# Kernel tuning notes

Hardware: AMD Instinct MI355X
Metric: run time of the kernel (lower is better)

Reference implementation:

```python
import jax, jax.numpy as jnp
import numpy as np

DIM = 2048
HID = 5632
ZERO_POINT = 128.0


def _qlinear(x, wq, scale):
    # wq: uint8-style codes stored as int32, shape [out, in]; scale: [out]
    W = (wq.astype(jnp.float32) - ZERO_POINT) * scale[:, None]  # dequant [out, in]
    return jnp.einsum('bsd,hd->bsh', x, W)


def setup_inputs() -> dict:
    key = jax.random.key(0)
    ks = jax.random.split(key, 7)
    B, S = 4, 2048
    # scale chosen so dequantized weights have ~1/sqrt(fan_in) magnitude
    sg = jax.random.uniform(ks[1], (HID,)) * (0.02 / np.sqrt(DIM)) + 1e-4
    su = jax.random.uniform(ks[3], (HID,)) * (0.02 / np.sqrt(DIM)) + 1e-4
    sd = jax.random.uniform(ks[5], (DIM,)) * (0.02 / np.sqrt(HID)) + 1e-4
    return {
        'x': jax.random.normal(ks[0], (B, S, DIM), dtype=jnp.float32),
        'wq_gate': jax.random.randint(ks[2], (HID, DIM), 0, 256, dtype=jnp.int32),
        's_gate': sg,
        'wq_up': jax.random.randint(ks[4], (HID, DIM), 0, 256, dtype=jnp.int32),
        's_up': su,
        'wq_down': jax.random.randint(ks[6], (DIM, HID), 0, 256, dtype=jnp.int32),
        's_down': sd,
    }


def reference(x, wq_gate, s_gate, wq_up, s_up, wq_down, s_down):
    gate = _qlinear(x, wq_gate, s_gate)          # [B, S, HID]
    gate = jax.nn.silu(gate)
    up = _qlinear(x, wq_up, s_up)                # [B, S, HID]
    return _qlinear(gate * up, wq_down, s_down)  # [B, S, DIM]
```

## Files before the change

kernel.cpp:

```cpp
#include <hip/hip_runtime.h>
#include <hip/hip_bf16.h>
#include <stdint.h>

#define DIM 2048
#define HID 5632
#define PDIM 2176

typedef __attribute__((ext_vector_type(8))) short short8;
typedef __attribute__((ext_vector_type(4))) float f32x4;
typedef __attribute__((ext_vector_type(4))) int int4v;
typedef __attribute__((ext_vector_type(4))) unsigned short ushort4v;

__device__ __forceinline__ unsigned short f32_to_bf16_rne(float f) {
    union { float f; unsigned u; } v; v.f = f;
    unsigned u = v.u;
    return (unsigned short)((u + 0x7FFFu + ((u >> 16) & 1u)) >> 16);
}

__device__ __forceinline__ void gload16(const void* g, void* l) {
    __builtin_amdgcn_global_load_lds(
        (const __attribute__((address_space(1))) void*)g,
        (__attribute__((address_space(3))) void*)l,
        16, 0, 0);
}

#define PH_OPEN \
    __builtin_amdgcn_sched_barrier(0); \
    __builtin_amdgcn_s_barrier(); \
    asm volatile("s_waitcnt lgkmcnt(0)" ::: "memory"); \
    __builtin_amdgcn_sched_barrier(0); \
    __builtin_amdgcn_s_setprio(1);
#define PH_CLOSE \
    __builtin_amdgcn_s_setprio(0); \
    __builtin_amdgcn_sched_barrier(0); \
    __builtin_amdgcn_s_barrier(); \
    __builtin_amdgcn_sched_barrier(0);
#define PH_CLOSE_VM(N) \
    __builtin_amdgcn_s_setprio(0); \
    __builtin_amdgcn_sched_barrier(0); \
    asm volatile("s_waitcnt vmcnt(" #N ")" ::: "memory"); \
    __builtin_amdgcn_sched_barrier(0); \
    __builtin_amdgcn_s_barrier(); \
    __builtin_amdgcn_sched_barrier(0);

__global__ void dequant_plain(const int* __restrict__ wq, const float* __restrict__ scale,
                              unsigned short* __restrict__ out, long total, int cols) {
    long n4 = total >> 2;
    long stride = (long)gridDim.x * blockDim.x;
    for (long i = (long)blockIdx.x * blockDim.x + threadIdx.x; i < n4; i += stride) {
        int4v c = ((const int4v*)wq)[i];
        int row = (int)((i << 2) / cols);
        float s = scale[row];
        ushort4v o;
        o.x = f32_to_bf16_rne(((float)c.x - 128.0f) * s);
        o.y = f32_to_bf16_rne(((float)c.y - 128.0f) * s);
        o.z = f32_to_bf16_rne(((float)c.z - 128.0f) * s);
        o.w = f32_to_bf16_rne(((float)c.w - 128.0f) * s);
        ((ushort4v*)out)[i] = o;
    }
}

__global__ void dequant_gateup(const int* __restrict__ wg, const float* __restrict__ sg,
                               const int* __restrict__ wu, const float* __restrict__ su,
                               unsigned short* __restrict__ out) {
    const long n4 = (long)HID * DIM / 4;
    const int CPR = PDIM / 4;
    long stride = (long)gridDim.x * blockDim.x;
    for (long i = (long)blockIdx.x * blockDim.x + threadIdx.x; i < n4; i += stride) {
        int r  = (int)(i >> 9);
        int c4 = (int)(i & 511);
        int rp = ((r >> 4) << 5) + (r & 15);
        float s1 = sg[r], s2 = su[r];
        int4v g = ((const int4v*)wg)[i];
        int4v u = ((const int4v*)wu)[i];
        ushort4v og, ou;
        og.x = f32_to_bf16_rne(((float)g.x - 128.0f) * s1);
        og.y = f32_to_bf16_rne(((float)g.y - 128.0f) * s1);
        og.z = f32_to_bf16_rne(((float)g.z - 128.0f) * s1);
        og.w = f32_to_bf16_rne(((float)g.w - 128.0f) * s1);
        ou.x = f32_to_bf16_rne(((float)u.x - 128.0f) * s2);
        ou.y = f32_to_bf16_rne(((float)u.y - 128.0f) * s2);
        ou.z = f32_to_bf16_rne(((float)u.z - 128.0f) * s2);
        ou.w = f32_to_bf16_rne(((float)u.w - 128.0f) * s2);
        ((ushort4v*)out)[(long)rp * CPR + c4]        = og;
        ((ushort4v*)out)[(long)(rp + 16) * CPR + c4] = ou;
    }
}

__global__ void cast_f32_bf16(const float* __restrict__ in, unsigned short* __restrict__ out, long n) {
    long n4 = n >> 2;
    const int CPR = PDIM / 4;
    long stride = (long)gridDim.x * blockDim.x;
    for (long i = (long)blockIdx.x * blockDim.x + threadIdx.x; i < n4; i += stride) {
        f32x4 v = ((const f32x4*)in)[i];
        int r  = (int)(i >> 9);
        int c4 = (int)(i & 511);
        ushort4v o;
        o.x = f32_to_bf16_rne(v[0]);
        o.y = f32_to_bf16_rne(v[1]);
        o.z = f32_to_bf16_rne(v[2]);
        o.w = f32_to_bf16_rne(v[3]);
        ((ushort4v*)out)[(long)r * CPR + c4] = o;
    }
}


#define GEMM_PROLOGUE_COMMON(Aptr, Bptr, LDA, LDB)                                   \
    const int tid  = threadIdx.x;                                                    \
    const int lane = tid & 63;                                                       \
    const int wid  = tid >> 6;                                                       \
    const int wr   = wid >> 2;                                                       \
    const int wc   = wid & 3;                                                        \
    const int m0   = blockIdx.x << 8;                                                \
    const int n0   = blockIdx.y << 8;                                                \
    const int lr   = lane & 15;                                                      \
    const int kg   = lane >> 4;                                                      \
    const int ck   = ((kg ^ ((lr >> 1) & 3)) << 3);                                  \
    const int aboff = (wr * 128 + lr) * 32;                                          \
    const int bboff = (wc * 64 + lr) * 32;                                           \
    int srow[2], scol[2], sdst[2];                                                   \
    _Pragma("unroll")                                                                \
    for (int l = 0; l < 2; ++l) {                                                    \
        int p = tid + (l << 9);                                                      \
        srow[l] = p >> 2;                                                            \
        scol[l] = (((p & 3) ^ ((p >> 3) & 3)) << 3);                                 \
        sdst[l] = p << 3;                                                            \
    }                                                                                \
    auto STAGE_A = [&](int t, int kh) {                                              \
        if (t < NT) {                                                                \
            unsigned short* dst = As + ((((t & 1) << 1) | kh) << 13);                \
            _Pragma("unroll")                                                        \
            for (int l = 0; l < 2; ++l)                                              \
                gload16(Aptr + (size_t)(m0 + srow[l]) * LDA + (t << 6) + (kh << 5) + scol[l], \
                        dst + sdst[l]);                                              \
        }                                                                            \
    };                                                                               \
    auto STAGE_B = [&](int t, int kh) {                                              \
        if (t < NT) {                                                                \
            unsigned short* dst = Bs + ((((t & 1) << 1) | kh) << 13);                \
            _Pragma("unroll")                                                        \
            for (int l = 0; l < 2; ++l)                                              \
                gload16(Bptr + (size_t)(n0 + srow[l]) * LDB + (t << 6) + (kh << 5) + scol[l], \
                        dst + sdst[l]);                                              \
        }                                                                            \
    };                                                                               \
    f32x4 acc[8][4];                                                                 \
    _Pragma("unroll")                                                                \
    for (int m = 0; m < 8; ++m)                                                      \
        _Pragma("unroll")                                                            \
        for (int n = 0; n < 4; ++n) acc[m][n] = (f32x4){0.f, 0.f, 0.f, 0.f};         \
                            \
    STAGE_A(0, 0); STAGE_B(0, 0);                                                    \
    STAGE_A(0, 1); STAGE_B(0, 1);                                                    \
    STAGE_A(1, 0); STAGE_B(1, 0);                                                    \
    asm volatile("s_waitcnt vmcnt(8)" ::: "memory");                                 \
    __builtin_amdgcn_s_barrier();

#define GEMM_KLOOP_BODY                                                              \
    for (int t = 0; t < NT; ++t) {                                                   \
        const int buf = t & 1;                                                       \
        const unsigned short* a0p = As + ((buf << 1) << 13) + aboff + ck;            \
        const unsigned short* a1p = As + (((buf << 1) | 1) << 13) + aboff + ck;      \
        const unsigned short* b0p = Bs + ((buf << 1) << 13) + bboff + ck;            \
        const unsigned short* b1p = Bs + (((buf << 1) | 1) << 13) + bboff + ck;      \
                                            \
        short8 b0[4], aL0[4];                                                        \
        _Pragma("unroll")                                                            \
        for (int n = 0; n < 4; ++n) b0[n] = *(const short8*)(b0p + (n << 9));        \
        _Pragma("unroll")                                                            \
        for (int m = 0; m < 4; ++m) aL0[m] = *(const short8*)(a0p + (m << 9));       \
        STAGE_A(t + 1, 1);                                                           \
        PH_OPEN                                                                      \
        _Pragma("unroll")                                                            \
        for (int m = 0; m < 4; ++m)                                                  \
            _Pragma("unroll")                                                        \
            for (int n = 0; n < 4; ++n)                                              \
                acc[m][n] = __builtin_amdgcn_mfma_f32_16x16x32_bf16(aL0[m], b0[n], acc[m][n], 0, 0, 0); \
        PH_CLOSE                                                                     \
                           \
        short8 aH0[4];                                                               \
        _Pragma("unroll")                                                            \
        for (int m = 0; m < 4; ++m) aH0[m] = *(const short8*)(a0p + ((m + 4) << 9)); \
        STAGE_B(t + 1, 1);                                                           \
        PH_OPEN                                                                      \
        _Pragma("unroll")                                                            \
        for (int m = 0; m < 4; ++m)                                                  \
            _Pragma("unroll")                                                        \
            for (int n = 0; n < 4; ++n)                                              \
                acc[m + 4][n] = __builtin_amdgcn_mfma_f32_16x16x32_bf16(aH0[m], b0[n], acc[m + 4][n], 0, 0, 0); \
        if (t < NT - 1) { PH_CLOSE_VM(8) } else { PH_CLOSE_VM(0) }                   \
                                            \
        short8 b1[4], aL1[4];                                                        \
        _Pragma("unroll")                                                            \
        for (int n = 0; n < 4; ++n) b1[n] = *(const short8*)(b1p + (n << 9));        \
        _Pragma("unroll")                                                            \
        for (int m = 0; m < 4; ++m) aL1[m] = *(const short8*)(a1p + (m << 9));       \
        STAGE_A(t + 2, 0);                                                           \
        PH_OPEN                                                                      \
        _Pragma("unroll")                                                            \
        for (int m = 0; m < 4; ++m)                                                  \
            _Pragma("unroll")                                                        \
            for (int n = 0; n < 4; ++n)                                              \
                acc[m][n] = __builtin_amdgcn_mfma_f32_16x16x32_bf16(aL1[m], b1[n], acc[m][n], 0, 0, 0); \
        PH_CLOSE                                                                     \
                         \
        short8 aH1[4];                                                               \
        _Pragma("unroll")                                                            \
        for (int m = 0; m < 4; ++m) aH1[m] = *(const short8*)(a1p + ((m + 4) << 9)); \
        STAGE_B(t + 2, 0);                                                           \
        PH_OPEN                                                                      \
        _Pragma("unroll")                                                            \
        for (int m = 0; m < 4; ++m)                                                  \
            _Pragma("unroll")                                                        \
            for (int n = 0; n < 4; ++n)                                              \
                acc[m + 4][n] = __builtin_amdgcn_mfma_f32_16x16x32_bf16(aH1[m], b1[n], acc[m + 4][n], 0, 0, 0); \
        if (t < NT - 2) { PH_CLOSE_VM(8) } else { PH_CLOSE_VM(4) }                   \
    }

__global__ __launch_bounds__(512, 1) void gemm_gateup(
    const unsigned short* __restrict__ X,
    const unsigned short* __restrict__ Wp,
    unsigned short* __restrict__ H)
{
    __shared__ __attribute__((aligned(16))) unsigned short As[2 * 2 * 8192];
    __shared__ __attribute__((aligned(16))) unsigned short Bs[2 * 2 * 8192];
    const int NT = DIM / 64;
    GEMM_PROLOGUE_COMMON(X, Wp, PDIM, PDIM)
    GEMM_KLOOP_BODY

    const int lg = lane >> 4;
    #pragma unroll
    for (int m = 0; m < 8; ++m) {
        #pragma unroll
        for (int i = 0; i < 2; ++i) {
            f32x4 g = acc[m][2 * i], u = acc[m][2 * i + 1];
            const int col = (blockIdx.y << 7) + wc * 32 + i * 16 + lr;
            #pragma unroll
            for (int e = 0; e < 4; ++e) {
                const int row = m0 + wr * 128 + m * 16 + lg * 4 + e;
                float gv = g[e];
                float sg = gv / (1.0f + __expf(-gv));
                H[(size_t)row * HID + col] = f32_to_bf16_rne(sg * u[e]);
            }
        }
    }
}

__global__ __launch_bounds__(512, 1) void gemm_down(
    const unsigned short* __restrict__ Hb,
    const unsigned short* __restrict__ Wd,
    float* __restrict__ Out)
{
    __shared__ __attribute__((aligned(16))) unsigned short As[2 * 2 * 8192];
    __shared__ __attribute__((aligned(16))) unsigned short Bs[2 * 2 * 8192];
    const int NT = HID / 64;
    GEMM_PROLOGUE_COMMON(Hb, Wd, HID, HID)
    GEMM_KLOOP_BODY

    const int lg = lane >> 4;
    #pragma unroll
    for (int m = 0; m < 8; ++m) {
        #pragma unroll
        for (int n = 0; n < 4; ++n) {
            const int col = n0 + wc * 64 + n * 16 + lr;
            #pragma unroll
            for (int e = 0; e < 4; ++e) {
                const int row = m0 + wr * 128 + m * 16 + lg * 4 + e;
                Out[(size_t)row * DIM + col] = acc[m][n][e];
            }
        }
    }
}

extern "C" void kernel_launch(void* const* d_in, const int* in_sizes, int n_in,
                              void* d_out, int out_size, void* d_ws, size_t ws_size,
                              hipStream_t stream) {
    const float* x      = (const float*)d_in[0];
    const int* wq_gate  = (const int*)d_in[1];
    const float* s_gate = (const float*)d_in[2];
    const int* wq_up    = (const int*)d_in[3];
    const float* s_up   = (const float*)d_in[4];
    const int* wq_down  = (const int*)d_in[5];
    const float* s_down = (const float*)d_in[6];
    float* out = (float*)d_out;

    const int M = in_sizes[0] / DIM;

    unsigned short* xb  = (unsigned short*)d_ws;
    unsigned short* wgu = xb + (size_t)M * PDIM;
    unsigned short* h   = wgu + (size_t)2 * HID * PDIM;

    cast_f32_bf16<<<2048, 256, 0, stream>>>(x, xb, (long)M * DIM);
    dequant_gateup<<<2048, 256, 0, stream>>>(wq_gate, s_gate, wq_up, s_up, wgu);

    gemm_gateup<<<dim3(M / 256, (2 * HID) / 256), 512, 0, stream>>>(xb, wgu, h);

    dequant_plain<<<2048, 256, 0, stream>>>(wq_down, s_down, wgu, (long)DIM * HID, HID);

    gemm_down<<<dim3(M / 256, DIM / 256), 512, 0, stream>>>(h, wgu, out);
}
```

Baseline: 600.9 us.

## Stage weights as uint8 and dequantize in registers, apply scales in epilogue

Weights are repacked to uint8 codes instead of pre-dequantized bf16. The GEMMs load half as many bytes per B tile into LDS and convert codes to bf16 (code minus zero point) in registers just before the MFMAs. Per-row scales are applied to the accumulators in the epilogue rather than baked into the weights. This cuts weight-repack write traffic and B-tile load bandwidth, at the cost of extra VALU conversion work inside the hot loop and a changed LDS swizzle and waitcnt schedule.

New measurement: 703.3 us. +17.0%, slower.

```diff
diff --git a/kernel.cpp b/kernel.cpp
--- a/kernel.cpp
+++ b/kernel.cpp
@@ -10,6 +10,8 @@
 typedef __attribute__((ext_vector_type(4))) float f32x4;
 typedef __attribute__((ext_vector_type(4))) int int4v;
 typedef __attribute__((ext_vector_type(4))) unsigned short ushort4v;
+typedef __attribute__((ext_vector_type(4))) unsigned char uchar4v;
+typedef __attribute__((ext_vector_type(2))) unsigned int u32x2;
 
 __device__ __forceinline__ unsigned short f32_to_bf16_rne(float f) {
     union { float f; unsigned u; } v; v.f = f;
@@ -24,6 +26,26 @@
         16, 0, 0);
 }
 
+__device__ __forceinline__ short8 deq8(u32x2 raw) {
+    float f[8];
+    #pragma unroll
+    for (int j = 0; j < 2; ++j) {
+        unsigned w = raw[j];
+        f[4*j+0] = (float)(w & 0xffu);
+        f[4*j+1] = (float)((w >> 8) & 0xffu);
+        f[4*j+2] = (float)((w >> 16) & 0xffu);
+        f[4*j+3] = (float)(w >> 24);
+    }
+    union { unsigned u[4]; short8 v; } cv;
+    #pragma unroll
+    for (int j = 0; j < 4; ++j) {
+        float lo = f[2*j]   - 128.0f;
+        float hi = f[2*j+1] - 128.0f;
+        asm("v_cvt_pk_bf16_f32 %0, %1, %2" : "=v"(cv.u[j]) : "v"(lo), "v"(hi));
+    }
+    return cv.v;
+}
+
 #define PH_OPEN \
     __builtin_amdgcn_sched_barrier(0); \
     __builtin_amdgcn_s_barrier(); \
@@ -43,47 +65,37 @@
     __builtin_amdgcn_s_barrier(); \
     __builtin_amdgcn_sched_barrier(0);
 
-__global__ void dequant_plain(const int* __restrict__ wq, const float* __restrict__ scale,
-                              unsigned short* __restrict__ out, long total, int cols) {
+__global__ void repack_plain(const int* __restrict__ wq, unsigned char* __restrict__ out, long total) {
     long n4 = total >> 2;
     long stride = (long)gridDim.x * blockDim.x;
     for (long i = (long)blockIdx.x * blockDim.x + threadIdx.x; i < n4; i += stride) {
         int4v c = ((const int4v*)wq)[i];
-        int row = (int)((i << 2) / cols);
-        float s = scale[row];
-        ushort4v o;
-        o.x = f32_to_bf16_rne(((float)c.x - 128.0f) * s);
-        o.y = f32_to_bf16_rne(((float)c.y - 128.0f) * s);
-        o.z = f32_to_bf16_rne(((float)c.z - 128.0f) * s);
-        o.w = f32_to_bf16_rne(((float)c.w - 128.0f) * s);
-        ((ushort4v*)out)[i] = o;
-    }
-}
-
-__global__ void dequant_gateup(const int* __restrict__ wg, const float* __restrict__ sg,
-                               const int* __restrict__ wu, const float* __restrict__ su,
-                               unsigned short* __restrict__ out) {
+        uchar4v o;
+        o.x = (unsigned char)c.x; o.y = (unsigned char)c.y;
+        o.z = (unsigned char)c.z; o.w = (unsigned char)c.w;
+        ((uchar4v*)out)[i] = o;
+    }
+}
+
+__global__ void repack_gateup(const int* __restrict__ wg, const float* __restrict__ sg,
+                              const int* __restrict__ wu, const float* __restrict__ su,
+                              unsigned char* __restrict__ out, float* __restrict__ sWp) {
     const long n4 = (long)HID * DIM / 4;
-    const int CPR = PDIM / 4;
     long stride = (long)gridDim.x * blockDim.x;
     for (long i = (long)blockIdx.x * blockDim.x + threadIdx.x; i < n4; i += stride) {
         int r  = (int)(i >> 9);
         int c4 = (int)(i & 511);
         int rp = ((r >> 4) << 5) + (r & 15);
-        float s1 = sg[r], s2 = su[r];
         int4v g = ((const int4v*)wg)[i];
         int4v u = ((const int4v*)wu)[i];
-        ushort4v og, ou;
-        og.x = f32_to_bf16_rne(((float)g.x - 128.0f) * s1);
-        og.y = f32_to_bf16_rne(((float)g.y - 128.0f) * s1);
-        og.z = f32_to_bf16_rne(((float)g.z - 128.0f) * s1);
-        og.w = f32_to_bf16_rne(((float)g.w - 128.0f) * s1);
-        ou.x = f32_to_bf16_rne(((float)u.x - 128.0f) * s2);
-        ou.y = f32_to_bf16_rne(((float)u.y - 128.0f) * s2);
-        ou.z = f32_to_bf16_rne(((float)u.z - 128.0f) * s2);
-        ou.w = f32_to_bf16_rne(((float)u.w - 128.0f) * s2);
-        ((ushort4v*)out)[(long)rp * CPR + c4]        = og;
-        ((ushort4v*)out)[(long)(rp + 16) * CPR + c4] = ou;
+        uchar4v og, ou;
+        og.x = (unsigned char)g.x; og.y = (unsigned char)g.y;
+        og.z = (unsigned char)g.z; og.w = (unsigned char)g.w;
+        ou.x = (unsigned char)u.x; ou.y = (unsigned char)u.y;
+        ou.z = (unsigned char)u.z; ou.w = (unsigned char)u.w;
+        *(uchar4v*)(out + (long)rp * PDIM + c4 * 4)        = og;
+        *(uchar4v*)(out + (long)(rp + 16) * PDIM + c4 * 4) = ou;
+        if (c4 == 0) { sWp[rp] = sg[r]; sWp[rp + 16] = su[r]; }
     }
 }
 
@@ -105,7 +117,7 @@
 }
 
 
-#define GEMM_PROLOGUE_COMMON(Aptr, Bptr, LDA, LDB)                                   \
+#define GEMM_PROLOGUE_COMMON(Aptr, Bptr, Sc, LDA, LDBB)                              \
     const int tid  = threadIdx.x;                                                    \
     const int lane = tid & 63;                                                       \
     const int wid  = tid >> 6;                                                       \
@@ -117,7 +129,8 @@
     const int kg   = lane >> 4;                                                      \
     const int ck   = ((kg ^ ((lr >> 1) & 3)) << 3);                                  \
     const int aboff = (wr * 128 + lr) * 32;                                          \
-    const int bboff = (wc * 64 + lr) * 32;                                           \
+    const int bcol8 = ((((kg >> 1) ^ ((lr >> 2) & 1)) << 4) | ((kg & 1) << 3));      \
+    const int bboff = (wc * 64 + lr) * 32 + bcol8;                                   \
     int srow[2], scol[2], sdst[2];                                                   \
     _Pragma("unroll")                                                                \
     for (int l = 0; l < 2; ++l) {                                                    \
@@ -126,6 +139,8 @@
         scol[l] = (((p & 3) ^ ((p >> 3) & 3)) << 3);                                 \
         sdst[l] = p << 3;                                                            \
     }                                                                                \
+    const int brow = tid >> 1;                                                       \
+    const int bsc  = (((tid & 1) ^ ((brow >> 2) & 1)) << 4);                         \
     auto STAGE_A = [&](int t, int kh) {                                              \
         if (t < NT) {                                                                \
             unsigned short* dst = As + ((((t & 1) << 1) | kh) << 13);                \
@@ -137,23 +152,23 @@
     };                                                                               \
     auto STAGE_B = [&](int t, int kh) {                                              \
         if (t < NT) {                                                                \
-            unsigned short* dst = Bs + ((((t & 1) << 1) | kh) << 13);                \
-            _Pragma("unroll")                                                        \
-            for (int l = 0; l < 2; ++l)                                              \
-                gload16(Bptr + (size_t)(n0 + srow[l]) * LDB + (t << 6) + (kh << 5) + scol[l], \
-                        dst + sdst[l]);                                              \
+            unsigned char* dst = Bs + ((((t & 1) << 1) | kh) << 13);                 \
+            gload16(Bptr + (size_t)(n0 + brow) * LDBB + (t << 6) + (kh << 5) + bsc,  \
+                    dst + (tid << 4));                                               \
         }                                                                            \
     };                                                                               \
+    float sB[4];                                                                     \
+    _Pragma("unroll")                                                                \
+    for (int n = 0; n < 4; ++n) sB[n] = Sc[n0 + wc * 64 + n * 16 + lr];              \
     f32x4 acc[8][4];                                                                 \
     _Pragma("unroll")                                                                \
     for (int m = 0; m < 8; ++m)                                                      \
         _Pragma("unroll")                                                            \
         for (int n = 0; n < 4; ++n) acc[m][n] = (f32x4){0.f, 0.f, 0.f, 0.f};         \
-                            \
     STAGE_A(0, 0); STAGE_B(0, 0);                                                    \
     STAGE_A(0, 1); STAGE_B(0, 1);                                                    \
     STAGE_A(1, 0); STAGE_B(1, 0);                                                    \
-    asm volatile("s_waitcnt vmcnt(8)" ::: "memory");                                 \
+    asm volatile("s_waitcnt vmcnt(6)" ::: "memory");                                 \
     __builtin_amdgcn_s_barrier();
 
 #define GEMM_KLOOP_BODY                                                              \
@@ -161,23 +176,25 @@
         const int buf = t & 1;                                                       \
         const unsigned short* a0p = As + ((buf << 1) << 13) + aboff + ck;            \
         const unsigned short* a1p = As + (((buf << 1) | 1) << 13) + aboff + ck;      \
-        const unsigned short* b0p = Bs + ((buf << 1) << 13) + bboff + ck;            \
-        const unsigned short* b1p = Bs + (((buf << 1) | 1) << 13) + bboff + ck;      \
-                                            \
-        short8 b0[4], aL0[4];                                                        \
-        _Pragma("unroll")                                                            \
-        for (int n = 0; n < 4; ++n) b0[n] = *(const short8*)(b0p + (n << 9));        \
+        const unsigned char*  bq0 = Bs + ((buf << 1) << 13) + bboff;                 \
+        const unsigned char*  bq1 = Bs + (((buf << 1) | 1) << 13) + bboff;           \
+                                        \
+        u32x2 b0r[4]; short8 aL0[4], b0[4];                                          \
+        _Pragma("unroll")                                                            \
+        for (int n = 0; n < 4; ++n) b0r[n] = *(const u32x2*)(bq0 + (n << 9));        \
         _Pragma("unroll")                                                            \
         for (int m = 0; m < 4; ++m) aL0[m] = *(const short8*)(a0p + (m << 9));       \
         STAGE_A(t + 1, 1);                                                           \
         PH_OPEN                                                                      \
         _Pragma("unroll")                                                            \
+        for (int n = 0; n < 4; ++n) b0[n] = deq8(b0r[n]);                            \
+        _Pragma("unroll")                                                            \
         for (int m = 0; m < 4; ++m)                                                  \
             _Pragma("unroll")                                                        \
             for (int n = 0; n < 4; ++n)                                              \
                 acc[m][n] = __builtin_amdgcn_mfma_f32_16x16x32_bf16(aL0[m], b0[n], acc[m][n], 0, 0, 0); \
         PH_CLOSE                                                                     \
-                           \
+                                                 \
         short8 aH0[4];                                                               \
         _Pragma("unroll")                                                            \
         for (int m = 0; m < 4; ++m) aH0[m] = *(const short8*)(a0p + ((m + 4) << 9)); \
@@ -188,22 +205,24 @@
             _Pragma("unroll")                                                        \
             for (int n = 0; n < 4; ++n)                                              \
                 acc[m + 4][n] = __builtin_amdgcn_mfma_f32_16x16x32_bf16(aH0[m], b0[n], acc[m + 4][n], 0, 0, 0); \
-        if (t < NT - 1) { PH_CLOSE_VM(8) } else { PH_CLOSE_VM(0) }                   \
-                                            \
-        short8 b1[4], aL1[4];                                                        \
-        _Pragma("unroll")                                                            \
-        for (int n = 0; n < 4; ++n) b1[n] = *(const short8*)(b1p + (n << 9));        \
+        if (t < NT - 1) { PH_CLOSE_VM(6) } else { PH_CLOSE_VM(0) }                   \
+                                        \
+        u32x2 b1r[4]; short8 aL1[4], b1[4];                                          \
+        _Pragma("unroll")                                                            \
+        for (int n = 0; n < 4; ++n) b1r[n] = *(const u32x2*)(bq1 + (n << 9));        \
         _Pragma("unroll")                                                            \
         for (int m = 0; m < 4; ++m) aL1[m] = *(const short8*)(a1p + (m << 9));       \
         STAGE_A(t + 2, 0);                                                           \
         PH_OPEN                                                                      \
         _Pragma("unroll")                                                            \
+        for (int n = 0; n < 4; ++n) b1[n] = deq8(b1r[n]);                            \
+        _Pragma("unroll")                                                            \
         for (int m = 0; m < 4; ++m)                                                  \
             _Pragma("unroll")                                                        \
             for (int n = 0; n < 4; ++n)                                              \
                 acc[m][n] = __builtin_amdgcn_mfma_f32_16x16x32_bf16(aL1[m], b1[n], acc[m][n], 0, 0, 0); \
         PH_CLOSE                                                                     \
-                         \
+                                                 \
         short8 aH1[4];                                                               \
         _Pragma("unroll")                                                            \
         for (int m = 0; m < 4; ++m) aH1[m] = *(const short8*)(a1p + ((m + 4) << 9)); \
@@ -214,18 +233,19 @@
             _Pragma("unroll")                                                        \
             for (int n = 0; n < 4; ++n)                                              \
                 acc[m + 4][n] = __builtin_amdgcn_mfma_f32_16x16x32_bf16(aH1[m], b1[n], acc[m + 4][n], 0, 0, 0); \
-        if (t < NT - 2) { PH_CLOSE_VM(8) } else { PH_CLOSE_VM(4) }                   \
+        if (t < NT - 2) { PH_CLOSE_VM(6) } else { PH_CLOSE_VM(3) }                   \
     }
 
 __global__ __launch_bounds__(512, 1) void gemm_gateup(
     const unsigned short* __restrict__ X,
-    const unsigned short* __restrict__ Wp,
+    const unsigned char* __restrict__ Wp8,
+    const float* __restrict__ sWp,
     unsigned short* __restrict__ H)
 {
     __shared__ __attribute__((aligned(16))) unsigned short As[2 * 2 * 8192];
-    __shared__ __attribute__((aligned(16))) unsigned short Bs[2 * 2 * 8192];
+    __shared__ __attribute__((aligned(16))) unsigned char  Bs[2 * 2 * 8192];
     const int NT = DIM / 64;
-    GEMM_PROLOGUE_COMMON(X, Wp, PDIM, PDIM)
+    GEMM_PROLOGUE_COMMON(X, Wp8, sWp, PDIM, PDIM)
     GEMM_KLOOP_BODY
 
     const int lg = lane >> 4;
@@ -238,9 +258,10 @@
             #pragma unroll
             for (int e = 0; e < 4; ++e) {
                 const int row = m0 + wr * 128 + m * 16 + lg * 4 + e;
-                float gv = g[e];
+                float gv = g[e] * sB[2 * i];
+                float uv = u[e] * sB[2 * i + 1];
                 float sg = gv / (1.0f + __expf(-gv));
-                H[(size_t)row * HID + col] = f32_to_bf16_rne(sg * u[e]);
+                H[(size_t)row * HID + col] = f32_to_bf16_rne(sg * uv);
             }
         }
     }
@@ -248,13 +269,14 @@
 
 __global__ __launch_bounds__(512, 1) void gemm_down(
     const unsigned short* __restrict__ Hb,
-    const unsigned short* __restrict__ Wd,
+    const unsigned char* __restrict__ Wd8,
+    const float* __restrict__ sD,
     float* __restrict__ Out)
 {
     __shared__ __attribute__((aligned(16))) unsigned short As[2 * 2 * 8192];
-    __shared__ __attribute__((aligned(16))) unsigned short Bs[2 * 2 * 8192];
+    __shared__ __attribute__((aligned(16))) unsigned char  Bs[2 * 2 * 8192];
     const int NT = HID / 64;
-    GEMM_PROLOGUE_COMMON(Hb, Wd, HID, HID)
+    GEMM_PROLOGUE_COMMON(Hb, Wd8, sD, HID, HID)
     GEMM_KLOOP_BODY
 
     const int lg = lane >> 4;
@@ -266,7 +288,7 @@
             #pragma unroll
             for (int e = 0; e < 4; ++e) {
                 const int row = m0 + wr * 128 + m * 16 + lg * 4 + e;
-                Out[(size_t)row * DIM + col] = acc[m][n][e];
+                Out[(size_t)row * DIM + col] = acc[m][n][e] * sB[n];
             }
         }
     }
@@ -286,16 +308,18 @@
 
     const int M = in_sizes[0] / DIM;
 
-    unsigned short* xb  = (unsigned short*)d_ws;
-    unsigned short* wgu = xb + (size_t)M * PDIM;
-    unsigned short* h   = wgu + (size_t)2 * HID * PDIM;
+    char* ws = (char*)d_ws;
+    unsigned short* xb   = (unsigned short*)ws;
+    unsigned char*  wgu8 = (unsigned char*)(ws + (size_t)M * PDIM * 2);
+    float*          sWp  = (float*)(ws + (size_t)M * PDIM * 2 + (size_t)2 * HID * PDIM);
+    unsigned short* h    = (unsigned short*)(ws + (size_t)M * PDIM * 2 + (size_t)2 * HID * PDIM + (size_t)2 * HID * 4);
 
     cast_f32_bf16<<<2048, 256, 0, stream>>>(x, xb, (long)M * DIM);
-    dequant_gateup<<<2048, 256, 0, stream>>>(wq_gate, s_gate, wq_up, s_up, wgu);
-
-    gemm_gateup<<<dim3(M / 256, (2 * HID) / 256), 512, 0, stream>>>(xb, wgu, h);
-
-    dequant_plain<<<2048, 256, 0, stream>>>(wq_down, s_down, wgu, (long)DIM * HID, HID);
-
-    gemm_down<<<dim3(M / 256, DIM / 256), 512, 0, stream>>>(h, wgu, out);
-}
+    repack_gateup<<<2048, 256, 0, stream>>>(wq_gate, s_gate, wq_up, s_up, wgu8, sWp);
+
+    gemm_gateup<<<dim3(M / 256, (2 * HID) / 256), 512, 0, stream>>>(xb, wgu8, sWp, h);
+
+    repack_plain<<<2048, 256, 0, stream>>>(wq_down, wgu8, (long)DIM * HID);
+
+    gemm_down<<<dim3(M / 256, DIM / 256), 512, 0, stream>>>(h, wgu8, s_down, out);
+}
```
